# Kernel optimization log

Hardware: AMD Instinct MI355X
Metric: run time of the kernel (lower is better)

Reference implementation:

```python
import jax, jax.numpy as jnp
from jax import lax
import numpy as np

B, T, N, C = 8, 12, 4000, 2
H, O = 64, 1


def setup_inputs() -> dict:
    key = jax.random.key(0)
    ks = jax.random.split(key, 10)
    s = 1.0 / np.sqrt(H)
    return {
        "x": jax.random.normal(ks[0], (B, T, N, C), jnp.float32),
        "adj": jax.random.uniform(ks[1], (N, N), jnp.float32) / N,  # row-normalized-ish
        "W_gcn": jax.random.normal(ks[2], (H, C), jnp.float32) * s,
        "b_gcn": jax.random.normal(ks[3], (H,), jnp.float32) * s,
        "W_ih": jax.random.normal(ks[4], (4 * H, H), jnp.float32) * s,
        "W_hh": jax.random.normal(ks[5], (4 * H, H), jnp.float32) * s,
        "b_ih": jax.random.normal(ks[6], (4 * H,), jnp.float32) * s,
        "b_hh": jax.random.normal(ks[7], (4 * H,), jnp.float32) * s,
        "W_out": jax.random.normal(ks[8], (O, H), jnp.float32) * s,
        "b_out": jax.random.normal(ks[9], (O,), jnp.float32) * s,
    }


def reference(x, adj, W_gcn, b_gcn, W_ih, W_hh, b_ih, b_hh, W_out, b_out):
    b, t, n, c = x.shape
    h_dim = W_hh.shape[1]
    # per-timestep graph aggregation + shared linear GCN + relu (all timesteps batched)
    xg = jnp.einsum('nm,btmc->btnc', adj, x)          # [B,T,N,C]
    g = jax.nn.relu(xg @ W_gcn.T + b_gcn)             # [B,T,N,H]
    # shared LSTM applied per node == one LSTM over flattened batch B*N
    seq = g.transpose(1, 0, 2, 3).reshape(t, b * n, h_dim)  # [T, B*N, H]

    def step(carry, xt):
        h, cst = carry
        gates = xt @ W_ih.T + b_ih + h @ W_hh.T + b_hh  # [B*N, 4H]
        i, f, gg, o = jnp.split(gates, 4, axis=-1)      # torch gate order i,f,g,o
        cst = jax.nn.sigmoid(f) * cst + jax.nn.sigmoid(i) * jnp.tanh(gg)
        h = jax.nn.sigmoid(o) * jnp.tanh(cst)
        return (h, cst), None

    init = (jnp.zeros((b * n, h_dim), x.dtype), jnp.zeros((b * n, h_dim), x.dtype))
    (h_last, _), _ = lax.scan(step, init, seq)
    h_last = h_last.reshape(b, n, h_dim)              # [B,N,H]
    return h_last @ W_out.T + b_out                   # [B,N,O]
```

## Files before the change

kernel.cpp:

```cpp
#include <hip/hip_runtime.h>

typedef _Float16 half8 __attribute__((ext_vector_type(8)));
typedef short short8v __attribute__((ext_vector_type(8)));
typedef unsigned short ushort4v __attribute__((ext_vector_type(4)));
typedef float floatx4 __attribute__((ext_vector_type(4)));

#define GLOBAL_AS __attribute__((address_space(1)))
#define LDS_AS __attribute__((address_space(3)))

__device__ __forceinline__ unsigned short f2bf(float f) {
  unsigned int u = __float_as_uint(f);
  unsigned int r = (u + 0x7FFFu + ((u >> 16) & 1u)) >> 16;
  return (unsigned short)r;
}
__device__ __forceinline__ float sigf(float x) {
  return __builtin_amdgcn_rcpf(1.f + __expf(-x));
}
__device__ __forceinline__ float tanhf_(float x) {
  return 1.f - 2.f * __builtin_amdgcn_rcpf(1.f + __expf(2.f * x));
}

__global__ __launch_bounds__(256) void prep_kernel(
    const float* __restrict__ x, const float* __restrict__ W_ih,
    const float* __restrict__ W_hh, unsigned short* __restrict__ XBT,
    unsigned short* __restrict__ Wt2) {
  int idx = blockIdx.x * 256 + threadIdx.x;
  if (idx < 96 * 1008) {
    int bt = idx / 1008;
    int mg = idx - bt * 1008;
    int m0 = mg * 4;
    int j0 = bt * 2;
    ushort4v c0, c1;
    if (m0 < 4000) {
      const float* px = x + ((size_t)bt * 4000 + m0) * 2;
      float4 v0 = *reinterpret_cast<const float4*>(px);
      float4 v1 = *reinterpret_cast<const float4*>(px + 4);
      c0[0] = f2bf(v0.x); c0[1] = f2bf(v0.z); c0[2] = f2bf(v1.x); c0[3] = f2bf(v1.z);
      c1[0] = f2bf(v0.y); c1[1] = f2bf(v0.w); c1[2] = f2bf(v1.y); c1[3] = f2bf(v1.w);
    } else {
      c0 = ushort4v{0, 0, 0, 0};
      c1 = ushort4v{0, 0, 0, 0};
    }
    *reinterpret_cast<ushort4v*>(&XBT[(size_t)j0 * 4032 + m0]) = c0;
    *reinterpret_cast<ushort4v*>(&XBT[(size_t)(j0 + 1) * 4032 + m0]) = c1;
  } else {
    int widx = idx - 96 * 1008;
    int j = widx >> 4, kq = widx & 15;
    const float* src = (kq < 8) ? (W_ih + j * 64 + kq * 8)
                                : (W_hh + j * 64 + (kq - 8) * 8);
    float4 v0 = *reinterpret_cast<const float4*>(src);
    float4 v1 = *reinterpret_cast<const float4*>(src + 4);
    half8 h;
    h[0] = (_Float16)v0.x; h[1] = (_Float16)v0.y; h[2] = (_Float16)v0.z; h[3] = (_Float16)v0.w;
    h[4] = (_Float16)v1.x; h[5] = (_Float16)v1.y; h[6] = (_Float16)v1.z; h[7] = (_Float16)v1.w;
    *reinterpret_cast<half8*>(&Wt2[j * 128 + kq * 8]) = h;
  }
}

__global__ __launch_bounds__(256, 2) void gcn_gemm_kernel(
    const float* __restrict__ adj, const unsigned short* __restrict__ XBT,
    float* __restrict__ XGP) {
  __shared__ float Ab[2][1024];
  __shared__ unsigned short Bb[2][12288];
  int tid = threadIdx.x;
  int w = tid >> 6, lane = tid & 63, l15 = lane & 15, kg = lane >> 4;
  int bid = blockIdx.x;
  int ch = bid / 250;
  int nb = bid - ch * 250;
  int n0 = nb * 16;
  int k0 = ch * 576;

  int a_row = (w << 2) + (lane >> 4);
  int a_g = lane & 15;
  int a_gx = (a_g & 8) | ((a_g ^ a_row) & 7);
  const float* aSrc = adj + (size_t)(n0 + a_row) * 4000 + (a_gx << 2);
  const float* aSrcT = adj + (size_t)(n0 + a_row) * 4000 + 3968 +
                       ((a_g < 8) ? (((a_g ^ a_row) & 7) << 2) : 0);
  const unsigned short* bSrc[6];
  int bj[6];
#pragma unroll
  for (int q = 0; q < 6; q++) {
    int ib = w * 6 + q;
    int j = ib * 8 + (lane >> 3);
    int g = lane & 7;
    bj[q] = ib * 512;
    bSrc[q] = XBT + (size_t)j * 4032 + ((g ^ (j & 7)) << 3);
  }

#define STAGE_K2(kt, buf)                                                      \
  {                                                                            \
    __builtin_amdgcn_global_load_lds((const GLOBAL_AS unsigned int*)(aSrc + (kt)), \
        (LDS_AS unsigned int*)&Ab[(buf)][w * 256], 16, 0, 0);                  \
    _Pragma("unroll")                                                          \
    for (int q = 0; q < 6; q++)                                                \
      __builtin_amdgcn_global_load_lds((const GLOBAL_AS unsigned int*)(bSrc[q] + (kt)), \
          (LDS_AS unsigned int*)&Bb[(buf)][bj[q]], 16, 0, 0);                  \
  }
#define STAGE_K2T(buf)                                                         \
  {                                                                            \
    __builtin_amdgcn_global_load_lds((const GLOBAL_AS unsigned int*)(aSrcT),   \
        (LDS_AS unsigned int*)&Ab[(buf)][w * 256], 16, 0, 0);                  \
    _Pragma("unroll")                                                          \
    for (int q = 0; q < 6; q++)                                                \
      __builtin_amdgcn_global_load_lds((const GLOBAL_AS unsigned int*)(bSrc[q] + 3968), \
          (LDS_AS unsigned int*)&Bb[(buf)][bj[q]], 16, 0, 0);                  \
  }

  floatx4 acc[3];
  acc[0] = acc[1] = acc[2] = floatx4{0.f, 0.f, 0.f, 0.f};
  int rowA = l15;
  int xA = (rowA & 7) << 2;
  int jb[3], xB[3];
#pragma unroll
  for (int ct = 0; ct < 3; ct++) {
    int j = w * 48 + ct * 16 + l15;
    jb[ct] = j * 64;
    xB[ct] = (j & 7) << 3;
  }

  STAGE_K2(k0, 0);
  for (int i = 0; i < 9; i++) {
    int cur = i & 1;
    int gtile = ch * 9 + i;
    if (i < 8) {
      if (ch * 9 + i + 1 == 62) { STAGE_K2T(cur ^ 1); }
      else                      { STAGE_K2(k0 + (i + 1) * 64, cur ^ 1); }
      asm volatile("s_waitcnt vmcnt(7)" ::: "memory");
    } else {
      asm volatile("s_waitcnt vmcnt(0)" ::: "memory");
    }
    __builtin_amdgcn_s_barrier();
    asm volatile("" ::: "memory");
    int kslim = (gtile == 62) ? 1 : 2;
    for (int ks = 0; ks < kslim; ks++) {
      int k0i = ks * 32 + kg * 8;
      float4 u = *reinterpret_cast<const float4*>(&Ab[cur][rowA * 64 + (k0i ^ xA)]);
      float4 v = *reinterpret_cast<const float4*>(&Ab[cur][rowA * 64 + ((k0i + 4) ^ xA)]);
      short8v af;
      af[0] = f2bf(u.x); af[1] = f2bf(u.y); af[2] = f2bf(u.z); af[3] = f2bf(u.w);
      af[4] = f2bf(v.x); af[5] = f2bf(v.y); af[6] = f2bf(v.z); af[7] = f2bf(v.w);
#pragma unroll
      for (int ct = 0; ct < 3; ct++) {
        short8v bf = *reinterpret_cast<const short8v*>(&Bb[cur][jb[ct] + (k0i ^ xB[ct])]);
        acc[ct] = __builtin_amdgcn_mfma_f32_16x16x32_bf16(af, bf, acc[ct], 0, 0, 0);
      }
    }
    __builtin_amdgcn_s_barrier();
  }
#pragma unroll
  for (int ct = 0; ct < 3; ct++) {
    int j = w * 48 + ct * 16 + l15;
#pragma unroll
    for (int e = 0; e < 4; e++) {
      int n = n0 + kg * 4 + e;
      XGP[(size_t)ch * 768000 + (size_t)j * 4000 + n] = acc[ct][e];
    }
  }
}

__global__ __launch_bounds__(256, 3) void lstm_kernel(
    const float* __restrict__ XGP, const unsigned short* __restrict__ Wt2,
    const float* __restrict__ W_gcn, const float* __restrict__ b_gcn,
    const float* __restrict__ b_ih, const float* __restrict__ b_hh,
    const float* __restrict__ W_out, const float* __restrict__ b_out,
    float* __restrict__ out) {
  __shared__ unsigned short A[32 * 128];
  __shared__ float xga[24 * 32];
  __shared__ float red[8 * 32];

  int tid = threadIdx.x;
  int w = tid >> 6, lane = tid & 63, l15 = lane & 15, kg = lane >> 4;
  int r0 = blockIdx.x * 32;
  int hidx = w * 16 + l15;

  half8 wf[4][4];
#pragma unroll
  for (int ct = 0; ct < 4; ct++) {
    int j = ct * 64 + hidx;
#pragma unroll
    for (int ks = 0; ks < 4; ks++)
      wf[ct][ks] = *reinterpret_cast<const half8*>(&Wt2[j * 128 + ks * 32 + kg * 8]);
  }
  float bI = b_ih[hidx] + b_hh[hidx];
  float bF = b_ih[64 + hidx] + b_hh[64 + hidx];
  float bG = b_ih[128 + hidx] + b_hh[128 + hidx];
  float bO = b_ih[192 + hidx] + b_hh[192 + hidx];
  float wg0 = W_gcn[2 * hidx], wg1 = W_gcn[2 * hidx + 1], bg = b_gcn[hidx];

  for (int i = tid; i < 32 * 128 / 2; i += 256)
    reinterpret_cast<unsigned int*>(A)[i] = 0u;
  for (int i = tid; i < 24 * 32; i += 256) {
    int row = i & 31, tc = i >> 5;
    int g = r0 + row;
    int b = g / 4000, n = g - b * 4000;
    size_t base = (size_t)(b * 24 + tc) * 4000 + n;
    float s = 0.f;
#pragma unroll
    for (int chh = 0; chh < 7; chh++) s += XGP[(size_t)chh * 768000 + base];
    xga[i] = s;
  }
  float creg[8];
#pragma unroll
  for (int i = 0; i < 8; i++) creg[i] = 0.f;
  __syncthreads();

  for (int t = 0; t < 12; t++) {
#pragma unroll
    for (int half = 0; half < 2; half++)
#pragma unroll
      for (int rr = 0; rr < 4; rr++) {
        int row = half * 16 + kg * 4 + rr;
        float xg0 = xga[(2 * t) * 32 + row];
        float xg1 = xga[(2 * t + 1) * 32 + row];
        float gv = fmaxf(xg0 * wg0 + xg1 * wg1 + bg, 0.f);
        _Float16 hv = (_Float16)gv;
        A[row * 128 + (hidx ^ ((row & 7) << 3))] = __builtin_bit_cast(unsigned short, hv);
      }
    __syncthreads();

    floatx4 acc[2][4];
#pragma unroll
    for (int rt = 0; rt < 2; rt++)
#pragma unroll
      for (int ct = 0; ct < 4; ct++) acc[rt][ct] = floatx4{0.f, 0.f, 0.f, 0.f};
#pragma unroll
    for (int rt = 0; rt < 2; rt++) {
      int row = rt * 16 + l15;
      int xr = (row & 7) << 3;
      half8 af[4];
#pragma unroll
      for (int ks = 0; ks < 4; ks++)
        af[ks] = *reinterpret_cast<const half8*>(&A[row * 128 + ((ks * 32 + kg * 8) ^ xr)]);
#pragma unroll
      for (int ks = 0; ks < 4; ks++)
#pragma unroll
        for (int ct = 0; ct < 4; ct++)
          acc[rt][ct] = __builtin_amdgcn_mfma_f32_16x16x32_f16(
              af[ks], wf[ct][ks], acc[rt][ct], 0, 0, 0);
    }
    __syncthreads();

#pragma unroll
    for (int rt = 0; rt < 2; rt++)
#pragma unroll
      for (int e = 0; e < 4; e++) {
        int row = rt * 16 + kg * 4 + e;
        float gi = acc[rt][0][e] + bI;
        float gf = acc[rt][1][e] + bF;
        float gg = acc[rt][2][e] + bG;
        float go = acc[rt][3][e] + bO;
        float c = sigf(gf) * creg[rt * 4 + e] + sigf(gi) * tanhf_(gg);
        creg[rt * 4 + e] = c;
        float h = sigf(go) * tanhf_(c);
        _Float16 hv = (_Float16)h;
        A[row * 128 + ((64 + hidx) ^ ((row & 7) << 3))] = __builtin_bit_cast(unsigned short, hv);
      }
  }
  __syncthreads();

  {
    int rg = tid & 31, kq = tid >> 5;
    float partial = 0.f;
#pragma unroll
    for (int i = 0; i < 8; i++) {
      int k = kq * 8 + i;
      float hv = (float)__builtin_bit_cast(
          _Float16, A[rg * 128 + ((64 + k) ^ ((rg & 7) << 3))]);
      partial += hv * W_out[k];
    }
    red[kq * 32 + rg] = partial;
  }
  __syncthreads();
  if (tid < 32) {
    float s = b_out[0];
#pragma unroll
    for (int i = 0; i < 8; i++) s += red[i * 32 + tid];
    out[r0 + tid] = s;
  }
}

extern "C" void kernel_launch(void* const* d_in, const int* in_sizes, int n_in,
                              void* d_out, int out_size, void* d_ws, size_t ws_size,
                              hipStream_t stream) {
  const float* x     = (const float*)d_in[0];
  const float* adj   = (const float*)d_in[1];
  const float* W_gcn = (const float*)d_in[2];
  const float* b_gcn = (const float*)d_in[3];
  const float* W_ih  = (const float*)d_in[4];
  const float* W_hh  = (const float*)d_in[5];
  const float* b_ih  = (const float*)d_in[6];
  const float* b_hh  = (const float*)d_in[7];
  const float* W_out = (const float*)d_in[8];
  const float* b_out = (const float*)d_in[9];
  float* outp = (float*)d_out;

  float* XGP = (float*)d_ws;
  unsigned short* XBT = (unsigned short*)((char*)d_ws + 21504000);
  unsigned short* Wt2 = (unsigned short*)((char*)d_ws + 23052288);

  prep_kernel<<<394, 256, 0, stream>>>(x, W_ih, W_hh, XBT, Wt2);
  gcn_gemm_kernel<<<1750, 256, 0, stream>>>(adj, XBT, XGP);
  lstm_kernel<<<1000, 256, 0, stream>>>(XGP, Wt2, W_gcn, b_gcn, b_ih, b_hh,
                                        W_out, b_out, outp);
}
```

Measured before the change: 195.9 us.

## Retile GCN GEMM to 64x192 with triple buffering and fold log2e into LSTM weights

The aggregation GEMM moves from 16-row tiles to 64-row by 192-column tiles with a 2x2 wave layout, 32-wide K steps and a three-stage LDS pipeline, so each adj row is reused more and far fewer blocks are launched. The partial-sum output layout becomes node-major, and the LSTM gather is updated to match. The LSTM folds log2(e) scaling into the fp16 weights and biases so gates can use exp2 directly, and it seeds the accumulators with the bias. Occupancy hints change (launch bounds 4 for the LSTM). Risks include the overlapping last tile at n0=3936, the larger GEMM register footprint, and fewer blocks to fill the device.

```diff
diff --git a/kernel.cpp b/kernel.cpp
--- a/kernel.cpp
+++ b/kernel.cpp
@@ -7,17 +7,13 @@
 
 #define GLOBAL_AS __attribute__((address_space(1)))
 #define LDS_AS __attribute__((address_space(3)))
+#define L2E 1.44269504f
+#define L2E2 2.88539008f
 
 __device__ __forceinline__ unsigned short f2bf(float f) {
   unsigned int u = __float_as_uint(f);
   unsigned int r = (u + 0x7FFFu + ((u >> 16) & 1u)) >> 16;
   return (unsigned short)r;
-}
-__device__ __forceinline__ float sigf(float x) {
-  return __builtin_amdgcn_rcpf(1.f + __expf(-x));
-}
-__device__ __forceinline__ float tanhf_(float x) {
-  return 1.f - 2.f * __builtin_amdgcn_rcpf(1.f + __expf(2.f * x));
 }
 
 __global__ __launch_bounds__(256) void prep_kernel(
@@ -46,13 +42,16 @@
   } else {
     int widx = idx - 96 * 1008;
     int j = widx >> 4, kq = widx & 15;
+    float scale = (j >= 128 && j < 192) ? L2E2 : L2E;
     const float* src = (kq < 8) ? (W_ih + j * 64 + kq * 8)
                                 : (W_hh + j * 64 + (kq - 8) * 8);
     float4 v0 = *reinterpret_cast<const float4*>(src);
     float4 v1 = *reinterpret_cast<const float4*>(src + 4);
     half8 h;
-    h[0] = (_Float16)v0.x; h[1] = (_Float16)v0.y; h[2] = (_Float16)v0.z; h[3] = (_Float16)v0.w;
-    h[4] = (_Float16)v1.x; h[5] = (_Float16)v1.y; h[6] = (_Float16)v1.z; h[7] = (_Float16)v1.w;
+    h[0] = (_Float16)(v0.x * scale); h[1] = (_Float16)(v0.y * scale);
+    h[2] = (_Float16)(v0.z * scale); h[3] = (_Float16)(v0.w * scale);
+    h[4] = (_Float16)(v1.x * scale); h[5] = (_Float16)(v1.y * scale);
+    h[6] = (_Float16)(v1.z * scale); h[7] = (_Float16)(v1.w * scale);
     *reinterpret_cast<half8*>(&Wt2[j * 128 + kq * 8]) = h;
   }
 }
@@ -60,105 +59,106 @@
 __global__ __launch_bounds__(256, 2) void gcn_gemm_kernel(
     const float* __restrict__ adj, const unsigned short* __restrict__ XBT,
     float* __restrict__ XGP) {
-  __shared__ float Ab[2][1024];
-  __shared__ unsigned short Bb[2][12288];
+  __shared__ float Ab[3][2048];
+  __shared__ unsigned short Bb[3][6144];
   int tid = threadIdx.x;
   int w = tid >> 6, lane = tid & 63, l15 = lane & 15, kg = lane >> 4;
+  int wr = w >> 1, wc = w & 1;
   int bid = blockIdx.x;
-  int ch = bid / 250;
-  int nb = bid - ch * 250;
-  int n0 = nb * 16;
+  int ch = bid / 63;
+  int nb = bid - ch * 63;
+  int n0 = (nb == 62) ? 3936 : nb * 64;
   int k0 = ch * 576;
-
-  int a_row = (w << 2) + (lane >> 4);
-  int a_g = lane & 15;
-  int a_gx = (a_g & 8) | ((a_g ^ a_row) & 7);
-  const float* aSrc = adj + (size_t)(n0 + a_row) * 4000 + (a_gx << 2);
-  const float* aSrcT = adj + (size_t)(n0 + a_row) * 4000 + 3968 +
-                       ((a_g < 8) ? (((a_g ^ a_row) & 7) << 2) : 0);
-  const unsigned short* bSrc[6];
-  int bj[6];
-#pragma unroll
-  for (int q = 0; q < 6; q++) {
-    int ib = w * 6 + q;
-    int j = ib * 8 + (lane >> 3);
-    int g = lane & 7;
-    bj[q] = ib * 512;
-    bSrc[q] = XBT + (size_t)j * 4032 + ((g ^ (j & 7)) << 3);
-  }
-
-#define STAGE_K2(kt, buf)                                                      \
+  int nt = (ch == 6) ? 17 : 18;
+
+  const float* aS[2];
+#pragma unroll
+  for (int l = 0; l < 2; l++) {
+    int gi = l * 256 + tid;
+    int row = gi >> 3, kq = gi & 7;
+    aS[l] = adj + (size_t)(n0 + row) * 4000 + k0 + ((kq ^ (row & 7)) << 2);
+  }
+  const unsigned short* bS[3];
+#pragma unroll
+  for (int q = 0; q < 3; q++) {
+    int gi = q * 256 + tid;
+    int j = gi >> 2, gp = gi & 3;
+    bS[q] = XBT + (size_t)j * 4032 + k0 + ((gp ^ ((j >> 1) & 3)) << 3);
+  }
+  int bOff[6];
+#pragma unroll
+  for (int ct = 0; ct < 6; ct++) {
+    int j = wc * 96 + ct * 16 + l15;
+    bOff[ct] = j * 32 + ((kg ^ ((j >> 1) & 3)) << 3);
+  }
+
+#define K2_ISSUE(tt, bf)                                                       \
   {                                                                            \
-    __builtin_amdgcn_global_load_lds((const GLOBAL_AS unsigned int*)(aSrc + (kt)), \
-        (LDS_AS unsigned int*)&Ab[(buf)][w * 256], 16, 0, 0);                  \
     _Pragma("unroll")                                                          \
-    for (int q = 0; q < 6; q++)                                                \
-      __builtin_amdgcn_global_load_lds((const GLOBAL_AS unsigned int*)(bSrc[q] + (kt)), \
-          (LDS_AS unsigned int*)&Bb[(buf)][bj[q]], 16, 0, 0);                  \
-  }
-#define STAGE_K2T(buf)                                                         \
-  {                                                                            \
-    __builtin_amdgcn_global_load_lds((const GLOBAL_AS unsigned int*)(aSrcT),   \
-        (LDS_AS unsigned int*)&Ab[(buf)][w * 256], 16, 0, 0);                  \
+    for (int l = 0; l < 2; l++)                                                \
+      __builtin_amdgcn_global_load_lds(                                        \
+          (const GLOBAL_AS unsigned int*)(aS[l] + (tt) * 32),                  \
+          (LDS_AS unsigned int*)&Ab[(bf)][l * 1024 + w * 256], 16, 0, 0);      \
     _Pragma("unroll")                                                          \
-    for (int q = 0; q < 6; q++)                                                \
-      __builtin_amdgcn_global_load_lds((const GLOBAL_AS unsigned int*)(bSrc[q] + 3968), \
-          (LDS_AS unsigned int*)&Bb[(buf)][bj[q]], 16, 0, 0);                  \
-  }
-
-  floatx4 acc[3];
-  acc[0] = acc[1] = acc[2] = floatx4{0.f, 0.f, 0.f, 0.f};
-  int rowA = l15;
-  int xA = (rowA & 7) << 2;
-  int jb[3], xB[3];
-#pragma unroll
-  for (int ct = 0; ct < 3; ct++) {
-    int j = w * 48 + ct * 16 + l15;
-    jb[ct] = j * 64;
-    xB[ct] = (j & 7) << 3;
-  }
-
-  STAGE_K2(k0, 0);
-  for (int i = 0; i < 9; i++) {
-    int cur = i & 1;
-    int gtile = ch * 9 + i;
-    if (i < 8) {
-      if (ch * 9 + i + 1 == 62) { STAGE_K2T(cur ^ 1); }
-      else                      { STAGE_K2(k0 + (i + 1) * 64, cur ^ 1); }
-      asm volatile("s_waitcnt vmcnt(7)" ::: "memory");
+    for (int q = 0; q < 3; q++)                                                \
+      __builtin_amdgcn_global_load_lds(                                        \
+          (const GLOBAL_AS unsigned int*)(bS[q] + (tt) * 32),                  \
+          (LDS_AS unsigned int*)&Bb[(bf)][q * 2048 + w * 512], 16, 0, 0);      \
+  }
+
+  floatx4 acc[2][6];
+#pragma unroll
+  for (int rt = 0; rt < 2; rt++)
+#pragma unroll
+    for (int ct = 0; ct < 6; ct++) acc[rt][ct] = floatx4{0.f, 0.f, 0.f, 0.f};
+
+  K2_ISSUE(0, 0);
+  K2_ISSUE(1, 1);
+  for (int t = 0; t < nt; t++) {
+    int bufc = t % 3;
+    if (t + 2 < nt) {
+      K2_ISSUE(t + 2, (t + 2) % 3);
+      asm volatile("s_waitcnt vmcnt(10)" ::: "memory");
+    } else if (t == nt - 2) {
+      asm volatile("s_waitcnt vmcnt(5)" ::: "memory");
     } else {
       asm volatile("s_waitcnt vmcnt(0)" ::: "memory");
     }
+    __builtin_amdgcn_sched_barrier(0);
     __builtin_amdgcn_s_barrier();
     asm volatile("" ::: "memory");
-    int kslim = (gtile == 62) ? 1 : 2;
-    for (int ks = 0; ks < kslim; ks++) {
-      int k0i = ks * 32 + kg * 8;
-      float4 u = *reinterpret_cast<const float4*>(&Ab[cur][rowA * 64 + (k0i ^ xA)]);
-      float4 v = *reinterpret_cast<const float4*>(&Ab[cur][rowA * 64 + ((k0i + 4) ^ xA)]);
+#pragma unroll
+    for (int rt = 0; rt < 2; rt++) {
+      int r = wr * 32 + rt * 16 + l15;
+      int rx = (r & 7) << 2;
+      float4 u = *reinterpret_cast<const float4*>(&Ab[bufc][r * 32 + ((kg * 8) ^ rx)]);
+      float4 v = *reinterpret_cast<const float4*>(&Ab[bufc][r * 32 + ((kg * 8 + 4) ^ rx)]);
       short8v af;
       af[0] = f2bf(u.x); af[1] = f2bf(u.y); af[2] = f2bf(u.z); af[3] = f2bf(u.w);
       af[4] = f2bf(v.x); af[5] = f2bf(v.y); af[6] = f2bf(v.z); af[7] = f2bf(v.w);
 #pragma unroll
-      for (int ct = 0; ct < 3; ct++) {
-        short8v bf = *reinterpret_cast<const short8v*>(&Bb[cur][jb[ct] + (k0i ^ xB[ct])]);
-        acc[ct] = __builtin_amdgcn_mfma_f32_16x16x32_bf16(af, bf, acc[ct], 0, 0, 0);
+      for (int ct = 0; ct < 6; ct++) {
+        short8v bf = *reinterpret_cast<const short8v*>(&Bb[bufc][bOff[ct]]);
+        acc[rt][ct] = __builtin_amdgcn_mfma_f32_16x16x32_bf16(af, bf, acc[rt][ct], 0, 0, 0);
       }
     }
     __builtin_amdgcn_s_barrier();
   }
-#pragma unroll
-  for (int ct = 0; ct < 3; ct++) {
-    int j = w * 48 + ct * 16 + l15;
-#pragma unroll
-    for (int e = 0; e < 4; e++) {
-      int n = n0 + kg * 4 + e;
-      XGP[(size_t)ch * 768000 + (size_t)j * 4000 + n] = acc[ct][e];
-    }
-  }
-}
-
-__global__ __launch_bounds__(256, 3) void lstm_kernel(
+
+  size_t chbase = (size_t)ch * 768000;
+#pragma unroll
+  for (int rt = 0; rt < 2; rt++)
+#pragma unroll
+    for (int ct = 0; ct < 6; ct++)
+#pragma unroll
+      for (int e = 0; e < 4; e++) {
+        int n = n0 + wr * 32 + rt * 16 + kg * 4 + e;
+        int j = wc * 96 + ct * 16 + l15;
+        XGP[chbase + (size_t)n * 192 + j] = acc[rt][ct][e];
+      }
+}
+
+__global__ __launch_bounds__(256, 4) void lstm_kernel(
     const float* __restrict__ XGP, const unsigned short* __restrict__ Wt2,
     const float* __restrict__ W_gcn, const float* __restrict__ b_gcn,
     const float* __restrict__ b_ih, const float* __restrict__ b_hh,
@@ -181,23 +181,23 @@
     for (int ks = 0; ks < 4; ks++)
       wf[ct][ks] = *reinterpret_cast<const half8*>(&Wt2[j * 128 + ks * 32 + kg * 8]);
   }
-  float bI = b_ih[hidx] + b_hh[hidx];
-  float bF = b_ih[64 + hidx] + b_hh[64 + hidx];
-  float bG = b_ih[128 + hidx] + b_hh[128 + hidx];
-  float bO = b_ih[192 + hidx] + b_hh[192 + hidx];
+  float bI = (b_ih[hidx] + b_hh[hidx]) * L2E;
+  float bF = (b_ih[64 + hidx] + b_hh[64 + hidx]) * L2E;
+  float bG = (b_ih[128 + hidx] + b_hh[128 + hidx]) * L2E2;
+  float bO = (b_ih[192 + hidx] + b_hh[192 + hidx]) * L2E;
   float wg0 = W_gcn[2 * hidx], wg1 = W_gcn[2 * hidx + 1], bg = b_gcn[hidx];
 
   for (int i = tid; i < 32 * 128 / 2; i += 256)
     reinterpret_cast<unsigned int*>(A)[i] = 0u;
   for (int i = tid; i < 24 * 32; i += 256) {
-    int row = i & 31, tc = i >> 5;
+    int row = i / 24, tc = i - row * 24;
     int g = r0 + row;
     int b = g / 4000, n = g - b * 4000;
-    size_t base = (size_t)(b * 24 + tc) * 4000 + n;
+    size_t base = (size_t)n * 192 + b * 24 + tc;
     float s = 0.f;
 #pragma unroll
     for (int chh = 0; chh < 7; chh++) s += XGP[(size_t)chh * 768000 + base];
-    xga[i] = s;
+    xga[tc * 32 + row] = s;
   }
   float creg[8];
 #pragma unroll
@@ -220,9 +220,12 @@
 
     floatx4 acc[2][4];
 #pragma unroll
-    for (int rt = 0; rt < 2; rt++)
-#pragma unroll
-      for (int ct = 0; ct < 4; ct++) acc[rt][ct] = floatx4{0.f, 0.f, 0.f, 0.f};
+    for (int rt = 0; rt < 2; rt++) {
+      acc[rt][0] = floatx4{bI, bI, bI, bI};
+      acc[rt][1] = floatx4{bF, bF, bF, bF};
+      acc[rt][2] = floatx4{bG, bG, bG, bG};
+      acc[rt][3] = floatx4{bO, bO, bO, bO};
+    }
 #pragma unroll
     for (int rt = 0; rt < 2; rt++) {
       int row = rt * 16 + l15;
@@ -245,13 +248,14 @@
 #pragma unroll
       for (int e = 0; e < 4; e++) {
         int row = rt * 16 + kg * 4 + e;
-        float gi = acc[rt][0][e] + bI;
-        float gf = acc[rt][1][e] + bF;
-        float gg = acc[rt][2][e] + bG;
-        float go = acc[rt][3][e] + bO;
-        float c = sigf(gf) * creg[rt * 4 + e] + sigf(gi) * tanhf_(gg);
+        float si = __builtin_amdgcn_rcpf(1.f + __builtin_amdgcn_exp2f(-acc[rt][0][e]));
+        float sf = __builtin_amdgcn_rcpf(1.f + __builtin_amdgcn_exp2f(-acc[rt][1][e]));
+        float tg = 1.f - 2.f * __builtin_amdgcn_rcpf(1.f + __builtin_amdgcn_exp2f(acc[rt][2][e]));
+        float so = __builtin_amdgcn_rcpf(1.f + __builtin_amdgcn_exp2f(-acc[rt][3][e]));
+        float c = sf * creg[rt * 4 + e] + si * tg;
         creg[rt * 4 + e] = c;
-        float h = sigf(go) * tanhf_(c);
+        float tc = 1.f - 2.f * __builtin_amdgcn_rcpf(1.f + __builtin_amdgcn_exp2f(L2E2 * c));
+        float h = so * tc;
         _Float16 hv = (_Float16)h;
         A[row * 128 + ((64 + hidx) ^ ((row & 7) << 3))] = __builtin_bit_cast(unsigned short, hv);
       }
@@ -299,7 +303,7 @@
   unsigned short* Wt2 = (unsigned short*)((char*)d_ws + 23052288);
 
   prep_kernel<<<394, 256, 0, stream>>>(x, W_ih, W_hh, XBT, Wt2);
-  gcn_gemm_kernel<<<1750, 256, 0, stream>>>(adj, XBT, XGP);
+  gcn_gemm_kernel<<<441, 256, 0, stream>>>(adj, XBT, XGP);
   lstm_kernel<<<1000, 256, 0, stream>>>(XGP, Wt2, W_gcn, b_gcn, b_ih, b_hh,
                                         W_out, b_out, outp);
 }
```

After: 243.6 us. +24.3%, slower.
